# Performance work log

Measured on AMD Instinct MI355X. Metric: run time of the kernel, lower is better.

## Reference

```python
import jax, jax.numpy as jnp
import numpy as np

D_MODEL = 1024
N_HEADS = 16


def setup_inputs() -> dict:
    key = jax.random.key(0)
    ks = jax.random.split(key, 7)
    s = 0.02
    x = jax.random.normal(ks[0], (4, 2048, D_MODEL), dtype=jnp.float32)
    Wq = jax.random.normal(ks[1], (D_MODEL, D_MODEL), dtype=jnp.float32) * s
    Wk = jax.random.normal(ks[2], (D_MODEL, D_MODEL), dtype=jnp.float32) * s
    Wv = jax.random.normal(ks[3], (D_MODEL, D_MODEL), dtype=jnp.float32) * s
    bq = jax.random.normal(ks[4], (D_MODEL,), dtype=jnp.float32) * s
    bk = jax.random.normal(ks[5], (D_MODEL,), dtype=jnp.float32) * s
    bv = jax.random.normal(ks[6], (D_MODEL,), dtype=jnp.float32) * s
    return {"x": x, "Wq": Wq, "bq": bq, "Wk": Wk, "bk": bk, "Wv": Wv, "bv": bv}


def reference(x, Wq, bq, Wk, bk, Wv, bv):
    B, S, D = x.shape
    H = N_HEADS
    hd = D // H
    # torch Linear: y = x @ W.T + b
    q = (x @ Wq.T + bq).reshape(B, S, H, hd).transpose(0, 2, 1, 3)  # [B,H,S,hd]
    k = (x @ Wk.T + bk).reshape(B, S, H, hd).transpose(0, 2, 1, 3)
    v = (x @ Wv.T + bv).reshape(B, S, H, hd).transpose(0, 2, 1, 3)
    # NOTE: source scales by sqrt(d_model), not sqrt(head_dim)
    scores = jnp.einsum('bhqd,bhkd->bhqk', q, k) / jnp.sqrt(jnp.float32(D))
    attn = jax.nn.softmax(scores, axis=-1)
    out = jnp.einsum('bhqk,bhkd->bhqd', attn, v)  # [B,H,S,hd]
    return out.transpose(0, 2, 1, 3).reshape(B, S, D)
```

## Files before the change

### kernel.cpp

```cpp
#include <hip/hip_runtime.h>
#include <hip/hip_bf16.h>

#define D_MODEL 1024
#define NHEADS  16
#define HD      64
#define BATCH   4
#define SEQ     2048

#define XELEMS (BATCH * SEQ * D_MODEL)
#define WELEMS (D_MODEL * D_MODEL)

typedef __attribute__((ext_vector_type(8))) short v8s;
typedef __attribute__((ext_vector_type(4))) float v4f;

using bf16 = __hip_bfloat16;

#define GLD_LDS(gp, lp) \
    __builtin_amdgcn_global_load_lds((const __attribute__((address_space(1))) void*)(gp), \
                                     (__attribute__((address_space(3))) void*)(lp), 16, 0, 0)

#if __has_builtin(__builtin_amdgcn_exp2f)
#define EXP2(x) __builtin_amdgcn_exp2f(x)
#else
#define EXP2(x) exp2f(x)
#endif

__device__ __forceinline__ unsigned int f2bf(float f) {
    union { float f; unsigned int u; } c; c.f = f;
    unsigned int u = c.u;
    u += 0x7fffu + ((u >> 16) & 1u);
    return u >> 16;
}

__device__ __forceinline__ unsigned int pack_bf16_hu(float lo, float hi) {
    unsigned int a = __float_as_uint(lo) + 0x8000u;
    unsigned int b = __float_as_uint(hi) + 0x8000u;
    return __builtin_amdgcn_perm(b, a, 0x07060302u);
}

__device__ __forceinline__ uint4 cvt8(const float* p) {
    float4 f0 = ((const float4*)p)[0];
    float4 f1 = ((const float4*)p)[1];
    uint4 r;
    r.x = f2bf(f0.x) | (f2bf(f0.y) << 16);
    r.y = f2bf(f0.z) | (f2bf(f0.w) << 16);
    r.z = f2bf(f1.x) | (f2bf(f1.y) << 16);
    r.w = f2bf(f1.z) | (f2bf(f1.w) << 16);
    return r;
}

__device__ __forceinline__ void qswap32(unsigned int &a, unsigned int &b) {
#if __has_builtin(__builtin_amdgcn_permlane32_swap)
    auto r = __builtin_amdgcn_permlane32_swap(a, b, false, false);
    a = (unsigned int)r[0]; b = (unsigned int)r[1];
#else
    unsigned int ax = (unsigned int)__shfl_xor((int)a, 32, 64);
    unsigned int bx = (unsigned int)__shfl_xor((int)b, 32, 64);
    if (threadIdx.x & 32) { a = bx; } else { b = ax; }
#endif
}
__device__ __forceinline__ void qswap16(unsigned int &a, unsigned int &b) {
#if __has_builtin(__builtin_amdgcn_permlane16_swap)
    auto r = __builtin_amdgcn_permlane16_swap(a, b, false, false);
    a = (unsigned int)r[0]; b = (unsigned int)r[1];
#else
    unsigned int ax = (unsigned int)__shfl_xor((int)a, 16, 64);
    unsigned int bx = (unsigned int)__shfl_xor((int)b, 16, 64);
    if (threadIdx.x & 16) { a = bx; } else { b = ax; }
#endif
}

__global__ void detect_dtype(const unsigned short* __restrict__ x16,
                             int* __restrict__ flag) {
    int lane = threadIdx.x;
    unsigned short v = x16[2 * lane];
    int e = (v >> 7) & 0xff;
    bool plaus = (e >= 90) && (e <= 141);
    unsigned long long m = __ballot(plaus);
    if (lane == 0) *flag = (__popcll(m) >= 48) ? 1 : 0;
}

__global__ __launch_bounds__(256) void convert_inputs(
    const void* __restrict__ x,
    const void* __restrict__ wq, const void* __restrict__ wk,
    const void* __restrict__ wv,
    const void* __restrict__ bq, const void* __restrict__ bk,
    const void* __restrict__ bv,
    bf16* __restrict__ xbf, bf16* __restrict__ wbf, bf16* __restrict__ bbf,
    const int* __restrict__ flag)
{
    const int isbf = *flag;
    long g = (long)blockIdx.x * 256 + threadIdx.x;
    const long xg = XELEMS / 8;
    const long wg = WELEMS / 8;
    const long bg = D_MODEL / 8;
    const void* src; bf16* dst; long off;
    if      (g < xg)                  { src = x;  dst = xbf;              off = g; }
    else if (g < xg + wg)             { src = wq; dst = wbf;              off = g - xg; }
    else if (g < xg + 2*wg)           { src = wk; dst = wbf + WELEMS;     off = g - xg - wg; }
    else if (g < xg + 3*wg)           { src = wv; dst = wbf + 2*WELEMS;   off = g - xg - 2*wg; }
    else if (g < xg + 3*wg + bg)      { src = bq; dst = bbf;              off = g - xg - 3*wg; }
    else if (g < xg + 3*wg + 2*bg)    { src = bk; dst = bbf + D_MODEL;    off = g - xg - 3*wg - bg; }
    else if (g < xg + 3*wg + 3*bg)    { src = bv; dst = bbf + 2*D_MODEL;  off = g - xg - 3*wg - 2*bg; }
    else return;
    uint4 r = isbf ? ((const uint4*)src)[off]
                   : cvt8((const float*)src + off * 8);
    ((uint4*)dst)[off] = r;
}

__global__ __launch_bounds__(256, 2) void qkv_gemm(
    const bf16* __restrict__ xbf, const bf16* __restrict__ wbf,
    const bf16* __restrict__ bbf,
    bf16* __restrict__ qout, bf16* __restrict__ kout, bf16* __restrict__ vout)
{
    __shared__ bf16 Atile[128 * 32];
    __shared__ bf16 Btile[128 * 32];

    const int z = blockIdx.z;
    const bf16* W    = wbf + (size_t)z * WELEMS;
    const bf16* bias = bbf + z * D_MODEL;
    bf16* out = (z == 0) ? qout : (z == 1) ? kout : vout;
    const float scale = (z == 0) ? (1.4426950408889634f / 32.0f) : 1.0f;

    const int tid  = threadIdx.x;
    const int lane = tid & 63;
    const int wave = tid >> 6;
    const int m0w  = (wave >> 1) * 64;
    const int n0w  = (wave & 1) * 64;
    const int m_base = blockIdx.x * 128;
    const int n_base = blockIdx.y * 128;

    const int lm   = lane & 15;
    const int quad = lane >> 4;
    const int lk   = quad * 8;

    v4f acc[4][4] = {};

    for (int k0 = 0; k0 < D_MODEL; k0 += 32) {
        __syncthreads();
        #pragma unroll
        for (int p = 0; p < 2; ++p) {
            int chunk = wave + 4 * p;
            int row   = chunk * 16 + (lane >> 2);
            const bf16* ga = xbf + (size_t)(m_base + row) * D_MODEL + k0 + (lane & 3) * 8;
            const bf16* gb = W   + (size_t)(n_base + row) * D_MODEL + k0 + (lane & 3) * 8;
            GLD_LDS(ga, Atile + chunk * 16 * 32);
            GLD_LDS(gb, Btile + chunk * 16 * 32);
        }
        __syncthreads();

        v8s afrag[4], bfrag[4];
        #pragma unroll
        for (int mt = 0; mt < 4; ++mt)
            afrag[mt] = *(const v8s*)(Atile + (m0w + mt * 16 + lm) * 32 + lk);
        #pragma unroll
        for (int nt = 0; nt < 4; ++nt)
            bfrag[nt] = *(const v8s*)(Btile + (n0w + nt * 16 + lm) * 32 + lk);
        #pragma unroll
        for (int mt = 0; mt < 4; ++mt)
            #pragma unroll
            for (int nt = 0; nt < 4; ++nt)
                acc[mt][nt] = __builtin_amdgcn_mfma_f32_16x16x32_bf16(
                    afrag[mt], bfrag[nt], acc[mt][nt], 0, 0, 0);
    }

    #pragma unroll
    for (int nt = 0; nt < 4; ++nt) {
        int n = n_base + n0w + nt * 16 + lm;
        float bb = __bfloat162float(bias[n]);
        int h = n >> 6, d = n & 63;
        #pragma unroll
        for (int mt = 0; mt < 4; ++mt) {
            if (z == 2) {
                int m = m_base + m0w + mt * 16 + quad * 4;
                int b = m >> 11, s = m & (SEQ - 1);
                float p0 = acc[mt][nt][0] + bb;
                float p1 = acc[mt][nt][1] + bb;
                float p2 = acc[mt][nt][2] + bb;
                float p3 = acc[mt][nt][3] + bb;
                uint2 pk;
                pk.x = pack_bf16_hu(p0, p1);
                pk.y = pack_bf16_hu(p2, p3);
                size_t bh = (size_t)(b * NHEADS + h);
                *(uint2*)(out + (((bh << 6) + d) << 11) + s) = pk;
            } else {
                #pragma unroll
                for (int r = 0; r < 4; ++r) {
                    int m = m_base + m0w + mt * 16 + quad * 4 + r;
                    int b = m >> 11, s = m & (SEQ - 1);
                    float vv = (acc[mt][nt][r] + bb) * scale;
                    size_t bh = (size_t)(b * NHEADS + h);
                    out[(((bh << 11) + s) << 6) + d] = __float2bfloat16(vv);
                }
            }
        }
    }
}

__global__ __launch_bounds__(256, 4) void attn(
    const bf16* __restrict__ q, const bf16* __restrict__ k,
    const bf16* __restrict__ vT, void* __restrict__ out,
    const int* __restrict__ flag)
{
    __shared__ bf16 Ks[2][8 * 512];
    __shared__ bf16 Vt[2][8 * 512];

    const int isbf = *flag;

    const int l   = blockIdx.x;
    const int idx = l >> 3;
    const int q0  = (idx & 15) * 128;
    const int bh  = (l & 7) + ((idx >> 4) << 3);
    const int b   = bh >> 4, h = bh & 15;
    const size_t head_base  = (size_t)bh * SEQ * HD;
    const size_t head_baseT = (size_t)bh * HD * SEQ;

    const int tid  = threadIdx.x;
    const int lane = tid & 63;
    const int wave = tid >> 6;
    const int lm   = lane & 15;
    const int quad = lane >> 4;

    const int slm = lane >> 2;
    const int sq  = lane & 3;
    const int fidx = (lm * 4 + quad) * 8;

    v8s aq[2][2];
    #pragma unroll
    for (int mt = 0; mt < 2; ++mt)
        #pragma unroll
        for (int kb = 0; kb < 2; ++kb)
            aq[mt][kb] = *(const v8s*)(q + head_base
                          + (size_t)(q0 + wave * 32 + mt * 16 + lm) * HD
                          + kb * 32 + quad * 8);

    float l_acc[2] = { 0.0f, 0.0f };
    v4f   O[2][4] = {};

    typedef union { v8s v; unsigned int u[4]; } AB;

    auto stage = [&](int bi, int kv0_) {
        #pragma unroll
        for (int j = 0; j < 2; ++j) {
            int c  = wave * 2 + j;
            int kt = c >> 1, kb = c & 1;
            const bf16* ga = k + head_base
                + (size_t)(kv0_ + kt * 16 + slm) * HD + kb * 32 + sq * 8;
            GLD_LDS(ga, &Ks[bi][c * 512]);
        }
        #pragma unroll
        for (int j = 0; j < 2; ++j) {
            int c  = wave * 2 + j;
            int g1 = c >> 2, dt = c & 3;
            const bf16* gv = vT + head_baseT
                + (size_t)(dt * 16 + slm) * SEQ + kv0_ + sq * 16 + g1 * 8;
            GLD_LDS(gv, &Vt[bi][c * 512]);
        }
    };

    stage(0, 0);
    __syncthreads();

    const int NT = SEQ / 64;
    for (int t = 0; t < NT; ++t) {
        const int cur = t & 1;
        if (t + 1 < NT) stage(cur ^ 1, (t + 1) * 64);

        v4f sc[4][2] = {};
        #pragma unroll
        for (int kb = 0; kb < 2; ++kb) {
            v8s kf[4];
            #pragma unroll
            for (int kt = 0; kt < 4; ++kt)
                kf[kt] = *(const v8s*)(&Ks[cur][(kt * 2 + kb) * 512] + fidx);
            #pragma unroll
            for (int kt = 0; kt < 4; ++kt)
                #pragma unroll
                for (int mt = 0; mt < 2; ++mt)
                    sc[kt][mt] = __builtin_amdgcn_mfma_f32_16x16x32_bf16(
                        kf[kt], aq[mt][kb], sc[kt][mt], 0, 0, 0);
        }

        unsigned int pw[2][4][2];
        #pragma unroll
        for (int mt = 0; mt < 2; ++mt) {
            #pragma unroll
            for (int kt = 0; kt < 4; ++kt) {
                float p0 = EXP2(sc[kt][mt][0]);
                float p1 = EXP2(sc[kt][mt][1]);
                float p2 = EXP2(sc[kt][mt][2]);
                float p3 = EXP2(sc[kt][mt][3]);
                l_acc[mt] += (p0 + p1) + (p2 + p3);
                pw[mt][kt][0] = pack_bf16_hu(p0, p1);
                pw[mt][kt][1] = pack_bf16_hu(p2, p3);
            }
        }

        #pragma unroll
        for (int mt = 0; mt < 2; ++mt)
            #pragma unroll
            for (int kt0 = 0; kt0 < 2; ++kt0)
                #pragma unroll
                for (int j = 0; j < 2; ++j)
                    qswap32(pw[mt][kt0][j], pw[mt][kt0 + 2][j]);
        #pragma unroll
        for (int mt = 0; mt < 2; ++mt)
            #pragma unroll
            for (int g1 = 0; g1 < 2; ++g1)
                #pragma unroll
                for (int j = 0; j < 2; ++j)
                    qswap16(pw[mt][2 * g1][j], pw[mt][2 * g1 + 1][j]);

        #pragma unroll
        for (int kk = 0; kk < 2; ++kk) {
            v8s bv8[4];
            #pragma unroll
            for (int dt = 0; dt < 4; ++dt)
                bv8[dt] = *(const v8s*)(&Vt[cur][(kk * 4 + dt) * 512] + fidx);
            #pragma unroll
            for (int mt = 0; mt < 2; ++mt) {
                AB a;
                a.u[0] = pw[mt][2 * kk + 0][0];
                a.u[1] = pw[mt][2 * kk + 0][1];
                a.u[2] = pw[mt][2 * kk + 1][0];
                a.u[3] = pw[mt][2 * kk + 1][1];
                #pragma unroll
                for (int dt = 0; dt < 4; ++dt)
                    O[mt][dt] = __builtin_amdgcn_mfma_f32_16x16x32_bf16(
                        a.v, bv8[dt], O[mt][dt], 0, 0, 0);
            }
        }

        __syncthreads();
    }

    float inv[2];
    #pragma unroll
    for (int mt = 0; mt < 2; ++mt) {
        float lsum = l_acc[mt];
        lsum += __shfl_xor(lsum, 16, 64);
        lsum += __shfl_xor(lsum, 32, 64);
        inv[mt] = 1.0f / lsum;
    }

    #pragma unroll
    for (int mt = 0; mt < 2; ++mt) {
        #pragma unroll
        for (int r = 0; r < 4; ++r) {
            float ir = __shfl(inv[mt], quad * 4 + r, 64);
            int s = q0 + wave * 32 + mt * 16 + quad * 4 + r;
            #pragma unroll
            for (int dt = 0; dt < 4; ++dt) {
                int d = dt * 16 + lm;
                size_t off = (size_t)(b * SEQ + s) * D_MODEL + h * HD + d;
                float val = O[mt][dt][r] * ir;
                if (isbf) ((bf16*)out)[off] = __float2bfloat16(val);
                else      ((float*)out)[off] = val;
            }
        }
    }
}

extern "C" void kernel_launch(void* const* d_in, const int* in_sizes, int n_in,
                              void* d_out, int out_size, void* d_ws, size_t ws_size,
                              hipStream_t stream) {
    const void* x  = d_in[0];
    const void* Wq = d_in[1];
    const void* bq = d_in[2];
    const void* Wk = d_in[3];
    const void* bk = d_in[4];
    const void* Wv = d_in[5];
    const void* bv = d_in[6];

    char* ws = (char*)d_ws;
    int*  flag = (int*)ws;
    bf16* wbf  = (bf16*)(ws + 256);
    bf16* bbf  = (bf16*)(ws + 256 + 3 * (size_t)WELEMS * 2);
    bf16* qws  = (bf16*)(ws + 256 + 3 * (size_t)WELEMS * 2 + 8192);
    const size_t per = (size_t)BATCH * NHEADS * SEQ * HD;
    bf16* kws = qws + per;
    bf16* vws = kws + per;

    bf16* xbf = (bf16*)d_out;

    detect_dtype<<<1, 64, 0, stream>>>((const unsigned short*)x, flag);

    const long ngroups = (long)XELEMS / 8 + 3L * (WELEMS / 8) + 3L * (D_MODEL / 8);
    convert_inputs<<<(int)((ngroups + 255) / 256), 256, 0, stream>>>(
        x, Wq, Wk, Wv, bq, bk, bv, xbf, wbf, bbf, flag);

    dim3 g1(64, 8, 3);
    qkv_gemm<<<g1, 256, 0, stream>>>(xbf, wbf, bbf, qws, kws, vws);

    attn<<<1024, 256, 0, stream>>>(qws, kws, vws, d_out, flag);
}
```

Baseline: 240.5 us.

## Double QKV GEMM K-step and swizzle LDS tiles into fragment-ordered chunks

The QKV projection GEMM now loads a 64-wide K slice per iteration instead of 32, halving the number of barrier pairs across the K loop. The LDS tiles are stored as 16x32 chunks in an order that matches the MFMA fragment reads, which should reduce LDS bank conflicts on the fragment loads. The launch bounds occupancy hint goes from 2 to 3 blocks per CU, which may tighten register allocation. The larger LDS footprint per block (32 KB) may limit how many blocks fit on a CU.

After: 234.5 us. 2.5% less time.

```diff
diff --git a/kernel.cpp b/kernel.cpp
--- a/kernel.cpp
+++ b/kernel.cpp
@@ -108,13 +108,13 @@
     ((uint4*)dst)[off] = r;
 }
 
-__global__ __launch_bounds__(256, 2) void qkv_gemm(
+__global__ __launch_bounds__(256, 3) void qkv_gemm(
     const bf16* __restrict__ xbf, const bf16* __restrict__ wbf,
     const bf16* __restrict__ bbf,
     bf16* __restrict__ qout, bf16* __restrict__ kout, bf16* __restrict__ vout)
 {
-    __shared__ bf16 Atile[128 * 32];
-    __shared__ bf16 Btile[128 * 32];
+    __shared__ bf16 Atile[16 * 512];
+    __shared__ bf16 Btile[16 * 512];
 
     const int z = blockIdx.z;
     const bf16* W    = wbf + (size_t)z * WELEMS;
@@ -132,36 +132,44 @@
 
     const int lm   = lane & 15;
     const int quad = lane >> 4;
-    const int lk   = quad * 8;
+
+    const int slm = lane >> 2;
+    const int sq  = lane & 3;
+    const int fidx = (lm * 4 + quad) * 8;
 
     v4f acc[4][4] = {};
 
-    for (int k0 = 0; k0 < D_MODEL; k0 += 32) {
+    for (int k0 = 0; k0 < D_MODEL; k0 += 64) {
         __syncthreads();
         #pragma unroll
-        for (int p = 0; p < 2; ++p) {
-            int chunk = wave + 4 * p;
-            int row   = chunk * 16 + (lane >> 2);
-            const bf16* ga = xbf + (size_t)(m_base + row) * D_MODEL + k0 + (lane & 3) * 8;
-            const bf16* gb = W   + (size_t)(n_base + row) * D_MODEL + k0 + (lane & 3) * 8;
-            GLD_LDS(ga, Atile + chunk * 16 * 32);
-            GLD_LDS(gb, Btile + chunk * 16 * 32);
+        for (int j = 0; j < 4; ++j) {
+            int c  = wave * 4 + j;
+            int rt = c >> 1, kb = c & 1;
+            const bf16* ga = xbf + (size_t)(m_base + rt * 16 + slm) * D_MODEL
+                                 + k0 + kb * 32 + sq * 8;
+            const bf16* gb = W   + (size_t)(n_base + rt * 16 + slm) * D_MODEL
+                                 + k0 + kb * 32 + sq * 8;
+            GLD_LDS(ga, Atile + c * 512);
+            GLD_LDS(gb, Btile + c * 512);
         }
         __syncthreads();
 
-        v8s afrag[4], bfrag[4];
-        #pragma unroll
-        for (int mt = 0; mt < 4; ++mt)
-            afrag[mt] = *(const v8s*)(Atile + (m0w + mt * 16 + lm) * 32 + lk);
-        #pragma unroll
-        for (int nt = 0; nt < 4; ++nt)
-            bfrag[nt] = *(const v8s*)(Btile + (n0w + nt * 16 + lm) * 32 + lk);
-        #pragma unroll
-        for (int mt = 0; mt < 4; ++mt)
+        #pragma unroll
+        for (int kb = 0; kb < 2; ++kb) {
+            v8s af[4], bf[4];
+            #pragma unroll
+            for (int mt = 0; mt < 4; ++mt)
+                af[mt] = *(const v8s*)(Atile + (((m0w >> 4) + mt) * 2 + kb) * 512 + fidx);
             #pragma unroll
             for (int nt = 0; nt < 4; ++nt)
-                acc[mt][nt] = __builtin_amdgcn_mfma_f32_16x16x32_bf16(
-                    afrag[mt], bfrag[nt], acc[mt][nt], 0, 0, 0);
+                bf[nt] = *(const v8s*)(Btile + (((n0w >> 4) + nt) * 2 + kb) * 512 + fidx);
+            #pragma unroll
+            for (int mt = 0; mt < 4; ++mt)
+                #pragma unroll
+                for (int nt = 0; nt < 4; ++nt)
+                    acc[mt][nt] = __builtin_amdgcn_mfma_f32_16x16x32_bf16(
+                        af[mt], bf[nt], acc[mt][nt], 0, 0, 0);
+        }
     }
 
     #pragma unroll
```
